# Optimization experiments

Hardware: AMD Instinct MI355X
Metric: run time of the kernel (lower is better)

The kernel has to match this reference:

```python
import jax, jax.numpy as jnp
import numpy as np

NQ = 4  # fixed by the encoder (4 rx encodings on wires 0..3)


def _apply_rx(state, theta, wire):
    # state: [B,2,2,2,2] complex64, theta: [B]
    c = jnp.cos(theta * 0.5).astype(jnp.complex64)
    s = (-1j) * jnp.sin(theta * 0.5).astype(jnp.complex64)
    g = jnp.stack([jnp.stack([c, s], -1), jnp.stack([s, c], -1)], -2)  # [B,2,2]
    st = jnp.moveaxis(state, wire + 1, 1)
    st = jnp.einsum('bij,bj...->bi...', g, st)
    return jnp.moveaxis(st, 1, wire + 1)


def _apply_cnot(state, ctrl, tgt):
    st = jnp.moveaxis(state, (ctrl + 1, tgt + 1), (1, 2))
    st = jnp.stack([st[:, 0], jnp.flip(st[:, 1], axis=1)], axis=1)
    return jnp.moveaxis(st, (1, 2), (ctrl + 1, tgt + 1))


def _qlayer(angles):
    # angles: [B,NQ] (encoder rx(x) + trainable rx(theta) fused: same-axis rotations add)
    # returns PauliZ expectation per wire: [B,NQ]
    B = angles.shape[0]
    state = jnp.zeros((B, 2 ** NQ), jnp.complex64).at[:, 0].set(1.0)
    state = state.reshape((B,) + (2,) * NQ)
    for w in range(NQ):
        state = _apply_rx(state, angles[:, w], w)
    for w in range(NQ):
        state = _apply_cnot(state, w, (w + 1) % NQ)
    p = state.real ** 2 + state.imag ** 2
    zs = []
    for w in range(NQ):
        pw = jnp.moveaxis(p, w + 1, 1).reshape(B, 2, -1).sum(-1)
        zs.append(pw[:, 0] - pw[:, 1])
    return jnp.stack(zs, axis=1)


def setup_inputs() -> dict:
    key = jax.random.key(0)
    ks = jax.random.split(key, 6)
    T, B, D = 128, 4096, 64
    fan = D + NQ
    inputs = jax.random.normal(ks[0], (T, B, D), jnp.float32)

    def lin(k):
        kw, kb = jax.random.split(k)
        W = jax.random.normal(kw, (NQ, fan), jnp.float32) / float(np.sqrt(fan))
        b = jax.random.normal(kb, (NQ,), jnp.float32) * 0.01
        return W, b

    Wf, bf = lin(ks[1])
    Wi, bi = lin(ks[2])
    Wu, bu = lin(ks[3])
    Wo, bo = lin(ks[4])
    thetas = jax.random.normal(ks[5], (4, NQ), jnp.float32) * 0.1  # rows: forget,input,update,output
    return dict(inputs=inputs, Wf=Wf, bf=bf, Wi=Wi, bi=bi, Wu=Wu, bu=bu,
                Wo=Wo, bo=bo, thetas=thetas)


def reference(inputs, Wf, bf, Wi, bi, Wu, bu, Wo, bo, thetas):
    B = inputs.shape[1]
    h0 = jnp.zeros((B, NQ), inputs.dtype)
    c0 = jnp.zeros((B, NQ), inputs.dtype)

    def step(carry, x):
        hx, cx = carry
        comb = jnp.concatenate([x, hx], axis=1)  # [B, D+NQ]
        f = jax.nn.sigmoid(_qlayer(comb @ Wf.T + bf + thetas[0]))
        i = jax.nn.sigmoid(_qlayer(comb @ Wi.T + bi + thetas[1]))
        g = jnp.tanh(_qlayer(comb @ Wu.T + bu + thetas[2]))
        o = jax.nn.sigmoid(_qlayer(comb @ Wo.T + bo + thetas[3]))
        cx_new = f * cx + i * g
        hx_new = o * jnp.tanh(cx_new)
        return (hx_new, cx_new), hx_new

    (hx, cx), stacked = jax.lax.scan(step, (h0, c0), inputs)
    # NOTE: original calls self.fcl.run(...) (shot-based Qiskit sim) on detached hx
    # and discards the result; it has no effect on outputs and is omitted.
    return stacked, hx, cx
```

## Files before the change

kernel.cpp:

```cpp
#include <hip/hip_runtime.h>
#include <cstdint>
#include <cstddef>

#define NQ 4
#define DIM 64
#define FAN 68
#define T_TOTAL 128
#define BATCH 4096

#define DPP_XOR1 0xB1
#define DPP_XOR2 0x4E

template <int CTRL>
__device__ __forceinline__ float dppq(float x) {
    return __int_as_float(
        __builtin_amdgcn_update_dpp(0, __float_as_int(x), CTRL, 0xF, 0xF, true));
}

__device__ __forceinline__ float fastrcp(float x) {
    return __builtin_amdgcn_rcpf(x);
}

__global__ __launch_bounds__(256) void qlstm_pre(
    const float* __restrict__ x,
    const float* __restrict__ Wf, const float* __restrict__ bf,
    const float* __restrict__ Wi, const float* __restrict__ bi,
    const float* __restrict__ Wu, const float* __restrict__ bu,
    const float* __restrict__ Wo, const float* __restrict__ bo,
    const float* __restrict__ thetas,
    float* __restrict__ pre,
    int nrows)
{
    int row = blockIdx.x * 256 + threadIdx.x;
    if (row >= nrows) return;

    const float4* xv = reinterpret_cast<const float4*>(x + (size_t)row * DIM);
    float4 xr[16];
#pragma unroll
    for (int j = 0; j < 16; ++j) xr[j] = xv[j];

    const float* Ws[4] = {Wf, Wi, Wu, Wo};
    const float* bs[4] = {bf, bi, bu, bo};

    float acc[16];
#pragma unroll
    for (int G = 0; G < 4; ++G) {
#pragma unroll
        for (int q = 0; q < NQ; ++q) {
            float a = bs[G][q] + thetas[G * NQ + q];
            const float4* wr = reinterpret_cast<const float4*>(Ws[G] + q * FAN);
#pragma unroll
            for (int j = 0; j < 16; ++j) {
                float4 w = wr[j];
                a = fmaf(xr[j].x, w.x, a);
                a = fmaf(xr[j].y, w.y, a);
                a = fmaf(xr[j].z, w.z, a);
                a = fmaf(xr[j].w, w.w, a);
            }
            acc[G * 4 + q] = a;
        }
    }

    float4* pv = reinterpret_cast<float4*>(pre + (size_t)row * 16);
#pragma unroll
    for (int k = 0; k < 4; ++k)
        pv[k] = make_float4(acc[4 * k], acc[4 * k + 1], acc[4 * k + 2], acc[4 * k + 3]);
}

__global__ __launch_bounds__(64) void qlstm_rec(
    const float* __restrict__ pre,
    const float* __restrict__ Wf, const float* __restrict__ Wi,
    const float* __restrict__ Wu, const float* __restrict__ Wo,
    float* __restrict__ out,
    float* __restrict__ state,
    int t0, int chunkT, int isFirst, int isLast)
{
    const int tid = threadIdx.x;
    const int g   = tid & 3;
    const int lb  = tid >> 2;
    const int b   = blockIdx.x * 16 + lb;

    const float* W = (g == 0) ? Wi : (g == 1) ? Wu : (g == 2) ? Wf : Wo;
    const int slot = (g == 0) ? 1  : (g == 1) ? 2  : (g == 2) ? 0  : 3;

    float wh[4][4];
#pragma unroll
    for (int q = 0; q < 4; ++q)
#pragma unroll
        for (int j = 0; j < 4; ++j)
            wh[q][j] = W[q * FAN + DIM + j];

    const bool is_u  = (g == 1);
    const bool is_g2 = (g == 2);
    const bool is_g3 = (g == 3);
    const bool hi    = (g >= 2);

    const float A  = is_u ? 2.0f : 1.0f;
    const float nB = is_u ? -2.0f : -1.0f;
    const float C  = is_u ? -1.0f : 0.0f;

    float h[4], c[4];
    if (isFirst) {
#pragma unroll
        for (int k = 0; k < 4; ++k) { h[k] = 0.0f; c[k] = 0.0f; }
    } else {
        float4 hv = *reinterpret_cast<const float4*>(state + (size_t)b * 4);
        float4 cv = *reinterpret_cast<const float4*>(state + (size_t)BATCH * 4 + (size_t)b * 4);
        h[0] = hv.x; h[1] = hv.y; h[2] = hv.z; h[3] = hv.w;
        c[0] = cv.x; c[1] = cv.y; c[2] = cv.z; c[3] = cv.w;
    }

    const char* pbase = (const char*)(pre + ((size_t)b * 16 + slot * 4));
    const size_t strideB = (size_t)BATCH * 16 * sizeof(float);

    float4 ring[4];
#pragma unroll
    for (int d = 0; d < 4; ++d) {
        int td = (d < chunkT) ? d : (chunkT - 1);
        ring[d] = *reinterpret_cast<const float4*>(pbase + (size_t)td * strideB);
    }

    for (int tt = 0; tt < chunkT; tt += 4) {
#pragma unroll
        for (int u = 0; u < 4; ++u) {
            int t = tt + u;
            if (t >= chunkT) break;
            float4 pv = ring[u];
            int tf = (t + 4 < chunkT) ? (t + 4) : (chunkT - 1);
            ring[u] = *reinterpret_cast<const float4*>(pbase + (size_t)tf * strideB);

            float a0 = pv.x, a1 = pv.y, a2 = pv.z, a3 = pv.w;
#pragma unroll
            for (int j = 0; j < 4; ++j) {
                a0 = fmaf(wh[0][j], h[j], a0);
                a1 = fmaf(wh[1][j], h[j], a1);
                a2 = fmaf(wh[2][j], h[j], a2);
                a3 = fmaf(wh[3][j], h[j], a3);
            }

            float c0 = __cosf(a0), c1 = __cosf(a1), c2 = __cosf(a2), c3 = __cosf(a3);
            float c12 = c1 * c2;
            float z[4];
            z[0] = c12 * c3;
            z[1] = c0 * c1;
            z[2] = c0 * c12;
            z[3] = z[2] * c3;

            float act[4];
#pragma unroll
            for (int k = 0; k < 4; ++k) {
                float e = __expf(nB * z[k]);
                act[k] = fmaf(A, fastrcp(1.0f + e), C);
            }

            float p1e[4], prod[4];
#pragma unroll
            for (int k = 0; k < 4; ++k) p1e[k] = dppq<DPP_XOR1>(act[k]);
#pragma unroll
            for (int k = 0; k < 4; ++k) {
                float xk = is_g3 ? p1e[k] : act[k];
                float yk = hi    ? c[k]   : p1e[k];
                prod[k] = xk * yk;
            }
#pragma unroll
            for (int k = 0; k < 4; ++k) {
                float p2e = dppq<DPP_XOR2>(prod[k]);
                c[k] = prod[k] + p2e;
            }
            float th[4];
#pragma unroll
            for (int k = 0; k < 4; ++k) {
                float e = __expf(-2.0f * c[k]);
                th[k] = fmaf(2.0f, fastrcp(1.0f + e), -1.0f);
            }
#pragma unroll
            for (int k = 0; k < 4; ++k) {
                float ov  = is_g2 ? p1e[k] : act[k];
                float p3e = dppq<DPP_XOR2>(ov);
                float Ov  = hi ? ov : p3e;
                h[k] = Ov * th[k];
            }

            float hg = (g == 0) ? h[0] : (g == 1) ? h[1] : (g == 2) ? h[2] : h[3];
            out[((size_t)(t0 + t) * BATCH + b) * 4 + g] = hg;
        }
    }

    float hg = (g == 0) ? h[0] : (g == 1) ? h[1] : (g == 2) ? h[2] : h[3];
    float cg = (g == 0) ? c[0] : (g == 1) ? c[1] : (g == 2) ? c[2] : c[3];
    state[(size_t)b * 4 + g] = hg;
    state[(size_t)BATCH * 4 + (size_t)b * 4 + g] = cg;

    if (isLast) {
        size_t tail = (size_t)T_TOTAL * BATCH * 4;
        out[tail + (size_t)b * 4 + g] = hg;
        out[tail + (size_t)BATCH * 4 + (size_t)b * 4 + g] = cg;
    }
}

extern "C" void kernel_launch(void* const* d_in, const int* in_sizes, int n_in,
                              void* d_out, int out_size, void* d_ws, size_t ws_size,
                              hipStream_t stream)
{
    const float* x  = (const float*)d_in[0];
    const float* Wf = (const float*)d_in[1];
    const float* bf = (const float*)d_in[2];
    const float* Wi = (const float*)d_in[3];
    const float* bi = (const float*)d_in[4];
    const float* Wu = (const float*)d_in[5];
    const float* bu = (const float*)d_in[6];
    const float* Wo = (const float*)d_in[7];
    const float* bo = (const float*)d_in[8];
    const float* th = (const float*)d_in[9];
    float* out = (float*)d_out;

    const size_t stateBytes = 2 * (size_t)BATCH * 4 * sizeof(float);
    const size_t perT       = (size_t)BATCH * 16 * sizeof(float);
    size_t avail = (ws_size > stateBytes) ? (ws_size - stateBytes) : 0;
    int chunkT = (int)(avail / perT);
    if (chunkT > T_TOTAL) chunkT = T_TOTAL;
    if (chunkT < 1) chunkT = 1;

    float* pre = (float*)d_ws;
    size_t stateOff = (ws_size - stateBytes) & ~(size_t)15;
    float* state = (float*)((char*)d_ws + stateOff);

    for (int t0 = 0; t0 < T_TOTAL; t0 += chunkT) {
        int ct = (T_TOTAL - t0 < chunkT) ? (T_TOTAL - t0) : chunkT;
        int nrows = ct * BATCH;
        qlstm_pre<<<(nrows + 255) / 256, 256, 0, stream>>>(
            x + (size_t)t0 * BATCH * DIM,
            Wf, bf, Wi, bi, Wu, bu, Wo, bo, th, pre, nrows);
        qlstm_rec<<<BATCH / 16, 64, 0, stream>>>(
            pre, Wf, Wi, Wu, Wo, out, state,
            t0, ct, (t0 == 0) ? 1 : 0, (t0 + ct >= T_TOTAL) ? 1 : 0);
    }
}
```

Before: 260.4 us.

## Spread recurrence over 16 lanes per batch row, one gate-qubit per lane

The recurrent kernel now gives each (gate, qubit) pair of a batch row its own lane, so 16 lanes cover one batch element instead of 4. The hidden-state matvec and cosine products are exchanged across lanes with DPP and ds_swizzle, and the grid grows to BATCH/4 blocks. This shortens the serial per-step dependency chain and raises wave-level parallelism for the latency-bound scan. In exchange it launches four times as many waves, adds cross-lane shuffles, and replaces each lane's float4 pre-activation loads with scalar loads.

```diff
diff --git a/kernel.cpp b/kernel.cpp
--- a/kernel.cpp
+++ b/kernel.cpp
@@ -10,11 +10,18 @@
 
 #define DPP_XOR1 0xB1
 #define DPP_XOR2 0x4E
+#define DPP_XOR3 0x1B
+#define DPP_ROR8 0x128
+#define SWZ_XOR4 0x101F
 
 template <int CTRL>
 __device__ __forceinline__ float dppq(float x) {
     return __int_as_float(
         __builtin_amdgcn_update_dpp(0, __float_as_int(x), CTRL, 0xF, 0xF, true));
+}
+
+__device__ __forceinline__ float swz_xor4(float x) {
+    return __int_as_float(__builtin_amdgcn_ds_swizzle(__float_as_int(x), SWZ_XOR4));
 }
 
 __device__ __forceinline__ float fastrcp(float x) {
@@ -76,48 +83,45 @@
     int t0, int chunkT, int isFirst, int isLast)
 {
     const int tid = threadIdx.x;
-    const int g   = tid & 3;
-    const int lb  = tid >> 2;
-    const int b   = blockIdx.x * 16 + lb;
-
-    const float* W = (g == 0) ? Wi : (g == 1) ? Wu : (g == 2) ? Wf : Wo;
-    const int slot = (g == 0) ? 1  : (g == 1) ? 2  : (g == 2) ? 0  : 3;
-
-    float wh[4][4];
-#pragma unroll
-    for (int q = 0; q < 4; ++q)
-#pragma unroll
-        for (int j = 0; j < 4; ++j)
-            wh[q][j] = W[q * FAN + DIM + j];
-
-    const bool is_u  = (g == 1);
-    const bool is_g2 = (g == 2);
-    const bool is_g3 = (g == 3);
-    const bool hi    = (g >= 2);
-
-    const float A  = is_u ? 2.0f : 1.0f;
+    const int grp = tid & 15;
+    const int G   = grp >> 2;
+    const int q   = grp & 3;
+    const int b   = blockIdx.x * 4 + (tid >> 4);
+
+    const float* W = (G == 0) ? Wi : (G == 1) ? Wu : (G == 2) ? Wf : Wo;
+    const int mG   = (G == 0) ? 1  : (G == 1) ? 2  : (G == 2) ? 0  : 3;
+
+    float w0 = W[q * FAN + DIM + 0];
+    float w1 = W[q * FAN + DIM + 1];
+    float w2 = W[q * FAN + DIM + 2];
+    float w3 = W[q * FAN + DIM + 3];
+    const int qA = q ^ 1, qB = q ^ 2, qC = q ^ 3;
+    float wS = (q  == 0) ? w0 : (q  == 1) ? w1 : (q  == 2) ? w2 : w3;
+    float wA = (qA == 0) ? w0 : (qA == 1) ? w1 : (qA == 2) ? w2 : w3;
+    float wB = (qB == 0) ? w0 : (qB == 1) ? w1 : (qB == 2) ? w2 : w3;
+    float wC = (qC == 0) ? w0 : (qC == 1) ? w1 : (qC == 2) ? w2 : w3;
+
+    const bool is_u = (G == 1);
+    const float Aa = is_u ?  2.0f :  1.0f;
     const float nB = is_u ? -2.0f : -1.0f;
-    const float C  = is_u ? -1.0f : 0.0f;
-
-    float h[4], c[4];
+    const float Cc = is_u ? -1.0f :  0.0f;
+
+    float hS, cS;
     if (isFirst) {
-#pragma unroll
-        for (int k = 0; k < 4; ++k) { h[k] = 0.0f; c[k] = 0.0f; }
+        hS = 0.0f; cS = 0.0f;
     } else {
-        float4 hv = *reinterpret_cast<const float4*>(state + (size_t)b * 4);
-        float4 cv = *reinterpret_cast<const float4*>(state + (size_t)BATCH * 4 + (size_t)b * 4);
-        h[0] = hv.x; h[1] = hv.y; h[2] = hv.z; h[3] = hv.w;
-        c[0] = cv.x; c[1] = cv.y; c[2] = cv.z; c[3] = cv.w;
-    }
-
-    const char* pbase = (const char*)(pre + ((size_t)b * 16 + slot * 4));
-    const size_t strideB = (size_t)BATCH * 16 * sizeof(float);
-
-    float4 ring[4];
+        hS = state[(size_t)b * 4 + q];
+        cS = state[(size_t)BATCH * 4 + (size_t)b * 4 + q];
+    }
+
+    const float* pptr = pre + ((size_t)b * 16 + mG * 4 + q);
+    const size_t strideT = (size_t)BATCH * 16;
+
+    float ring[4];
 #pragma unroll
     for (int d = 0; d < 4; ++d) {
         int td = (d < chunkT) ? d : (chunkT - 1);
-        ring[d] = *reinterpret_cast<const float4*>(pbase + (size_t)td * strideB);
+        ring[d] = pptr[(size_t)td * strideT];
     }
 
     for (int tt = 0; tt < chunkT; tt += 4) {
@@ -125,76 +129,64 @@
         for (int u = 0; u < 4; ++u) {
             int t = tt + u;
             if (t >= chunkT) break;
-            float4 pv = ring[u];
+            float p = ring[u];
             int tf = (t + 4 < chunkT) ? (t + 4) : (chunkT - 1);
-            ring[u] = *reinterpret_cast<const float4*>(pbase + (size_t)tf * strideB);
-
-            float a0 = pv.x, a1 = pv.y, a2 = pv.z, a3 = pv.w;
-#pragma unroll
-            for (int j = 0; j < 4; ++j) {
-                a0 = fmaf(wh[0][j], h[j], a0);
-                a1 = fmaf(wh[1][j], h[j], a1);
-                a2 = fmaf(wh[2][j], h[j], a2);
-                a3 = fmaf(wh[3][j], h[j], a3);
-            }
-
-            float c0 = __cosf(a0), c1 = __cosf(a1), c2 = __cosf(a2), c3 = __cosf(a3);
-            float c12 = c1 * c2;
-            float z[4];
-            z[0] = c12 * c3;
-            z[1] = c0 * c1;
-            z[2] = c0 * c12;
-            z[3] = z[2] * c3;
-
-            float act[4];
-#pragma unroll
-            for (int k = 0; k < 4; ++k) {
-                float e = __expf(nB * z[k]);
-                act[k] = fmaf(A, fastrcp(1.0f + e), C);
-            }
-
-            float p1e[4], prod[4];
-#pragma unroll
-            for (int k = 0; k < 4; ++k) p1e[k] = dppq<DPP_XOR1>(act[k]);
-#pragma unroll
-            for (int k = 0; k < 4; ++k) {
-                float xk = is_g3 ? p1e[k] : act[k];
-                float yk = hi    ? c[k]   : p1e[k];
-                prod[k] = xk * yk;
-            }
-#pragma unroll
-            for (int k = 0; k < 4; ++k) {
-                float p2e = dppq<DPP_XOR2>(prod[k]);
-                c[k] = prod[k] + p2e;
-            }
-            float th[4];
-#pragma unroll
-            for (int k = 0; k < 4; ++k) {
-                float e = __expf(-2.0f * c[k]);
-                th[k] = fmaf(2.0f, fastrcp(1.0f + e), -1.0f);
-            }
-#pragma unroll
-            for (int k = 0; k < 4; ++k) {
-                float ov  = is_g2 ? p1e[k] : act[k];
-                float p3e = dppq<DPP_XOR2>(ov);
-                float Ov  = hi ? ov : p3e;
-                h[k] = Ov * th[k];
-            }
-
-            float hg = (g == 0) ? h[0] : (g == 1) ? h[1] : (g == 2) ? h[2] : h[3];
-            out[((size_t)(t0 + t) * BATCH + b) * 4 + g] = hg;
+            ring[u] = pptr[(size_t)tf * strideT];
+
+            float hA = dppq<DPP_XOR1>(hS);
+            float hB = dppq<DPP_XOR2>(hS);
+            float hC = dppq<DPP_XOR3>(hS);
+
+            float a = p;
+            a = fmaf(wS, hS, a);
+            a = fmaf(wA, hA, a);
+            a = fmaf(wB, hB, a);
+            a = fmaf(wC, hC, a);
+
+            float cg = __cosf(a);
+
+            float cA = dppq<DPP_XOR1>(cg);
+            float cB = dppq<DPP_XOR2>(cg);
+            float cC = dppq<DPP_XOR3>(cg);
+            float s0 = (q == 0) ? 1.0f : cg;
+            float s1 = (q == 2) ? 1.0f : cA;
+            float s2 = (q == 1) ? 1.0f : cB;
+            float s3 = (q == 1) ? 1.0f : cC;
+            float z  = (s0 * s1) * (s2 * s3);
+
+            float e   = __expf(nB * z);
+            float act = fmaf(Aa, fastrcp(1.0f + e), Cc);
+
+            float partner = swz_xor4(act);
+
+            float xm = (G == 3) ? partner : act;
+            float ym = (G >= 2) ? cS : partner;
+            float prod = xm * ym;
+
+            float cn = prod + dppq<DPP_ROR8>(prod);
+            cS = cn;
+
+            float e2  = __expf(-2.0f * cn);
+            float tnh = fmaf(2.0f, fastrcp(1.0f + e2), -1.0f);
+
+            float tmpO = (G == 2) ? partner : act;
+            float OvH  = dppq<DPP_ROR8>(tmpO);
+            float Ov   = (G < 2) ? OvH : tmpO;
+
+            hS = Ov * tnh;
+
+            if (G == 0)
+                out[((size_t)(t0 + t) * BATCH + b) * 4 + q] = hS;
         }
     }
 
-    float hg = (g == 0) ? h[0] : (g == 1) ? h[1] : (g == 2) ? h[2] : h[3];
-    float cg = (g == 0) ? c[0] : (g == 1) ? c[1] : (g == 2) ? c[2] : c[3];
-    state[(size_t)b * 4 + g] = hg;
-    state[(size_t)BATCH * 4 + (size_t)b * 4 + g] = cg;
+    if (G == 0) state[(size_t)b * 4 + q] = hS;
+    if (G == 1) state[(size_t)BATCH * 4 + (size_t)b * 4 + q] = cS;
 
     if (isLast) {
         size_t tail = (size_t)T_TOTAL * BATCH * 4;
-        out[tail + (size_t)b * 4 + g] = hg;
-        out[tail + (size_t)BATCH * 4 + (size_t)b * 4 + g] = cg;
+        if (G == 0) out[tail + (size_t)b * 4 + q] = hS;
+        if (G == 1) out[tail + (size_t)BATCH * 4 + (size_t)b * 4 + q] = cS;
     }
 }
 
@@ -231,7 +223,7 @@
         qlstm_pre<<<(nrows + 255) / 256, 256, 0, stream>>>(
             x + (size_t)t0 * BATCH * DIM,
             Wf, bf, Wi, bi, Wu, bu, Wo, bo, th, pre, nrows);
-        qlstm_rec<<<BATCH / 16, 64, 0, stream>>>(
+        qlstm_rec<<<BATCH / 4, 64, 0, stream>>>(
             pre, Wf, Wi, Wu, Wo, out, state,
             t0, ct, (t0 == 0) ? 1 : 0, (t0 + ct >= T_TOTAL) ? 1 : 0);
     }
```

Result: slower. 265.8 us (+2.1%).
